# Kernel tuning notes

Measured on AMD Instinct MI355X. Metric: run time of the kernel, lower is better.

Reference implementation:

```python
import jax, jax.numpy as jnp
import numpy as np

N_EMBD = 2048
N_HEAD = 16
HEAD_DIM = N_EMBD // N_HEAD
MAX_SEQ = 2048
ROPE_BASE = 10000.0


def _build_rope_cache(seq_len, head_dim, base):
    theta = 1.0 / (base ** (jnp.arange(0, head_dim, 2, dtype=jnp.float32) / head_dim))
    idx_theta = jnp.arange(seq_len, dtype=jnp.float32)[:, None] * theta[None, :]  # [T, hd/2]
    return jnp.cos(idx_theta), jnp.sin(idx_theta)


def _apply_rope(x, cos, sin):
    # x: [B, T, H, hd]; interleaved (even, odd) pairing along last dim
    B, T, H, hd = x.shape
    xf = x.astype(jnp.float32).reshape(B, T, H, hd // 2, 2)
    x0, x1 = xf[..., 0], xf[..., 1]
    c = cos[None, :T, None, :]
    s = sin[None, :T, None, :]
    out = jnp.stack([x0 * c - x1 * s, x1 * c + x0 * s], axis=-1)
    return out.reshape(B, T, H, hd).astype(x.dtype)


def setup_inputs() -> dict:
    key = jax.random.key(0)
    k1, k2, k3 = jax.random.split(key, 3)
    x = jax.random.normal(k1, (2, 2048, N_EMBD), dtype=jnp.float32)
    # torch Linear(D, 3D, bias=False): y = x @ W.T ; store as [D, 3D] for x @ W
    scale = 1.0 / np.sqrt(N_EMBD)
    w_attn = jax.random.normal(k2, (N_EMBD, 3 * N_EMBD), dtype=jnp.float32) * scale
    w_proj = jax.random.normal(k3, (N_EMBD, N_EMBD), dtype=jnp.float32) * scale
    return {"x": x, "w_attn": w_attn, "w_proj": w_proj}


def reference(x, w_attn, w_proj):
    B, T, D = x.shape
    cos, sin = _build_rope_cache(MAX_SEQ, HEAD_DIM, ROPE_BASE)
    qkv = x @ w_attn                                   # [B, T, 3D]
    q, k, v = jnp.split(qkv, 3, axis=-1)
    q = q.reshape(B, T, N_HEAD, HEAD_DIM)
    k = k.reshape(B, T, N_HEAD, HEAD_DIM)
    v = v.reshape(B, T, N_HEAD, HEAD_DIM)
    q = _apply_rope(q, cos, sin)
    k = _apply_rope(k, cos, sin)
    # non-causal SDPA (original calls F.sdpa without is_causal)
    scale = 1.0 / jnp.sqrt(jnp.asarray(HEAD_DIM, dtype=q.dtype))
    scores = jnp.einsum("bqhd,bkhd->bhqk", q, k) * scale
    attn = jax.nn.softmax(scores, axis=-1)
    y = jnp.einsum("bhqk,bkhd->bqhd", attn, v).reshape(B, T, D)
    return y @ w_proj
```

## Files before the change

kernel.cpp:

```cpp
#include <hip/hip_runtime.h>
#include <cstdint>
#include <cstddef>

typedef __attribute__((ext_vector_type(8))) short bf16x8;
typedef __attribute__((ext_vector_type(8))) unsigned short us8;
typedef __attribute__((ext_vector_type(4))) float f32x4;

#define TSEQ 2048

__device__ __forceinline__ unsigned short f2bf(float f) {
  union { float f; uint32_t u; } v; v.f = f;
  uint32_t u = v.u;
  uint32_t r = (u + 0x7FFFu + ((u >> 16) & 1u)) >> 16;
  return (unsigned short)r;
}
__device__ __forceinline__ unsigned short f2bf_trunc(float f) {
  union { float f; uint32_t u; } v; v.f = f;
  return (unsigned short)(v.u >> 16);
}
__device__ __forceinline__ float bf2f(unsigned short h) {
  union { uint32_t u; float f; } v; v.u = ((uint32_t)h) << 16;
  return v.f;
}

__device__ __forceinline__ void async16(const void* g, void* l) {
  __builtin_amdgcn_global_load_lds(
      (const __attribute__((address_space(1))) unsigned int*)g,
      (__attribute__((address_space(3))) unsigned int*)l,
      16, 0, 0);
}

__global__ __launch_bounds__(256) void cvt_x(
    const float* __restrict__ in, unsigned short* __restrict__ out)
{
  const size_t i = ((size_t)blockIdx.x * 256 + threadIdx.x) * 16;
  f32x4 a0 = *(const f32x4*)(in + i);
  f32x4 a1 = *(const f32x4*)(in + i + 4);
  f32x4 a2 = *(const f32x4*)(in + i + 8);
  f32x4 a3 = *(const f32x4*)(in + i + 12);
  us8 lo, hi;
#pragma unroll
  for (int j = 0; j < 4; j++) {
    lo[j] = f2bf(a0[j]); lo[j + 4] = f2bf(a1[j]);
    hi[j] = f2bf(a2[j]); hi[j + 4] = f2bf(a3[j]);
  }
  *(us8*)(out + i) = lo;
  *(us8*)(out + i + 8) = hi;
}

__global__ __launch_bounds__(256) void transpose_w(
    const float* __restrict__ in, unsigned short* __restrict__ out,
    int R, int C)
{
  __shared__ unsigned short tile[32][33];
  const int bx = blockIdx.x * 32;
  const int by = blockIdx.y * 32;
  const int tx = threadIdx.x & 31;
  const int ty = threadIdx.x >> 5;
#pragma unroll
  for (int r = ty; r < 32; r += 8)
    tile[r][tx] = f2bf(in[(size_t)(by + r) * C + bx + tx]);
  __syncthreads();
#pragma unroll
  for (int r = ty; r < 32; r += 8)
    out[(size_t)(bx + r) * R + by + tx] = tile[tx][r];
}

template <int CF32>
__global__ __launch_bounds__(256) void gemm_bt(
    const unsigned short* __restrict__ A,
    const unsigned short* __restrict__ Bt,
    void* __restrict__ Cv,
    int M, int N, int K, int ldc)
{
  __shared__ unsigned short As[2][128 * 32];
  __shared__ unsigned short Bs[2][128 * 32];
  const int tid  = threadIdx.x;
  const int lane = tid & 63;
  const int w    = tid >> 6;
  const int m0   = blockIdx.y * 128;
  const int n0   = blockIdx.x * 128;
  const int wm   = (w & 1) * 64;
  const int wn   = (w >> 1) * 64;

  const int srow = lane >> 2;
  const int scol = (lane & 3) * 8;
  const unsigned short* ga0 = A  + (size_t)(m0 + w * 16 + srow) * K + scol;
  const unsigned short* ga1 = ga0 + (size_t)64 * K;
  const unsigned short* gb0 = Bt + (size_t)(n0 + w * 16 + srow) * K + scol;
  const unsigned short* gb1 = gb0 + (size_t)64 * K;

  f32x4 acc[4][4];
#pragma unroll
  for (int i = 0; i < 4; i++)
#pragma unroll
    for (int j = 0; j < 4; j++) acc[i][j] = (f32x4){0.f, 0.f, 0.f, 0.f};

  const int frow = lane & 15;
  const int fcol = (lane >> 4) * 8;

  for (int kt = 0; kt < K; kt += 64) {
    __syncthreads();
    async16(ga0 + kt,      &As[0][w * 512]);
    async16(ga1 + kt,      &As[0][(4 + w) * 512]);
    async16(ga0 + kt + 32, &As[1][w * 512]);
    async16(ga1 + kt + 32, &As[1][(4 + w) * 512]);
    async16(gb0 + kt,      &Bs[0][w * 512]);
    async16(gb1 + kt,      &Bs[0][(4 + w) * 512]);
    async16(gb0 + kt + 32, &Bs[1][w * 512]);
    async16(gb1 + kt + 32, &Bs[1][(4 + w) * 512]);
    __syncthreads();

#pragma unroll
    for (int h = 0; h < 2; h++) {
      bf16x8 af[4], bfr[4];
#pragma unroll
      for (int i = 0; i < 4; i++)
        af[i] = *(const bf16x8*)&As[h][(wm + i * 16 + frow) * 32 + fcol];
#pragma unroll
      for (int i = 0; i < 4; i++)
        bfr[i] = *(const bf16x8*)&Bs[h][(wn + i * 16 + frow) * 32 + fcol];
#pragma unroll
      for (int mi = 0; mi < 4; mi++)
#pragma unroll
        for (int ni = 0; ni < 4; ni++)
          acc[mi][ni] = __builtin_amdgcn_mfma_f32_16x16x32_bf16(
              af[mi], bfr[ni], acc[mi][ni], 0, 0, 0);
    }
  }

  const int crow0 = m0 + wm + (lane >> 4) * 4;
  const int ccol0 = n0 + wn + (lane & 15);
  if (CF32) {
    float* Cf = (float*)Cv;
#pragma unroll
    for (int mi = 0; mi < 4; mi++)
#pragma unroll
      for (int i = 0; i < 4; i++) {
        const int row = crow0 + mi * 16 + i;
#pragma unroll
        for (int ni = 0; ni < 4; ni++)
          Cf[(size_t)row * ldc + ccol0 + ni * 16] = acc[mi][ni][i];
      }
  } else {
    unsigned short* Cb = (unsigned short*)Cv;
#pragma unroll
    for (int mi = 0; mi < 4; mi++)
#pragma unroll
      for (int i = 0; i < 4; i++) {
        const int row = crow0 + mi * 16 + i;
#pragma unroll
        for (int ni = 0; ni < 4; ni++)
          Cb[(size_t)row * ldc + ccol0 + ni * 16] = f2bf(acc[mi][ni][i]);
      }
  }
}

__global__ __launch_bounds__(256) void rope_qk(unsigned short* __restrict__ qkv)
{
  const int p   = blockIdx.x * 256 + threadIdx.x;
  const int row = p >> 11;
  const int col = (p & 2047) * 2;
  const int t   = row & (TSEQ - 1);
  const int hd  = col & 127;
  const float theta = exp2f((float)hd * -0.1038102531f);
  const float ang   = (float)t * theta;
  float s, c;
  sincosf(ang, &s, &c);
  const float sc = (col < 2048) ? 0.08838834764831845f : 1.0f;
  uint32_t* ptr = (uint32_t*)(qkv + (size_t)row * 6144 + col);
  const uint32_t u = *ptr;
  const float x0 = bf2f((unsigned short)(u & 0xffffu));
  const float x1 = bf2f((unsigned short)(u >> 16));
  const float o0 = (x0 * c - x1 * s) * sc;
  const float o1 = (x1 * c + x0 * s) * sc;
  *ptr = (uint32_t)f2bf(o0) | ((uint32_t)f2bf(o1) << 16);
}

__global__ __launch_bounds__(256) void repack_v(
    const unsigned short* __restrict__ qkv, unsigned short* __restrict__ Vtg)
{
  __shared__ unsigned short tile[32][33];
  const int tt = blockIdx.x * 32;
  const int dd = blockIdx.y * 32;
  const int bh = blockIdx.z;
  const int b  = bh >> 4, h = bh & 15;
  const int tx = threadIdx.x & 31;
  const int ty = threadIdx.x >> 5;
#pragma unroll
  for (int r = ty; r < 32; r += 8)
    tile[r][tx] = qkv[(size_t)(b * TSEQ + tt + r) * 6144 + 4096 + h * 128 + dd + tx];
  __syncthreads();
#pragma unroll
  for (int r = ty; r < 32; r += 8)
    Vtg[(size_t)bh * 262144 + (size_t)(dd + r) * TSEQ + tt + tx] = tile[tx][r];
}

__global__ __launch_bounds__(256) void attn(
    const unsigned short* __restrict__ qkv,
    const unsigned short* __restrict__ Vtg,
    unsigned short* __restrict__ y)
{
  __shared__ unsigned short Ks[64 * 136];
  __shared__ unsigned short Vs[144 * 72];
  __shared__ unsigned short Ps[4][32 * 72];

  const int tid  = threadIdx.x;
  const int lane = tid & 63;
  const int w    = tid >> 6;
  const int q0   = blockIdx.x * 128;
  const int h    = blockIdx.y;
  const int b    = blockIdx.z;
  const int bh   = b * 16 + h;
  const int quad = lane >> 4;
  const int l15  = lane & 15;
  const int kq   = quad * 8;

  for (int idx = tid; idx < 16 * 72; idx += 256)
    Vs[128 * 72 + idx] = (idx < 72) ? (unsigned short)0x3F80 : (unsigned short)0;

  bf16x8 qa[2][4];
#pragma unroll
  for (int mt = 0; mt < 2; mt++) {
    const unsigned short* gQ =
        qkv + (size_t)(b * TSEQ + q0 + w * 32 + mt * 16 + l15) * 6144 + h * 128 + kq;
#pragma unroll
    for (int dc = 0; dc < 4; dc++) qa[mt][dc] = *(const bf16x8*)(gQ + dc * 32);
  }

  f32x4 ot[2][9];
#pragma unroll
  for (int mt = 0; mt < 2; mt++)
#pragma unroll
    for (int nt = 0; nt < 9; nt++) ot[mt][nt] = (f32x4){0.f, 0.f, 0.f, 0.f};

  const int krow = tid >> 2;
  const int kd   = (tid & 3) * 32;
  const unsigned short* gK = qkv + (size_t)(b * TSEQ) * 6144 + 2048 + h * 128 + kd;
  const int vd = tid >> 1;
  const int vc = (tid & 1) * 32;
  const unsigned short* gVt = Vtg + (size_t)bh * 262144 + (size_t)vd * TSEQ + vc;

  us8 kreg[4], vreg[4];
  {
    const unsigned short* pk = gK + (size_t)krow * 6144;
#pragma unroll
    for (int j = 0; j < 4; j++) kreg[j] = *(const us8*)(pk + j * 8);
#pragma unroll
    for (int j = 0; j < 4; j++) vreg[j] = *(const us8*)(gVt + j * 8);
  }

  for (int kb = 0; kb < TSEQ; kb += 64) {
    __syncthreads();
#pragma unroll
    for (int j = 0; j < 4; j++)
      *(us8*)&Ks[krow * 136 + kd + j * 8] = kreg[j];
#pragma unroll
    for (int j = 0; j < 4; j++)
      *(us8*)&Vs[vd * 72 + vc + j * 8] = vreg[j];
    __syncthreads();

    if (kb + 64 < TSEQ) {
      const unsigned short* pk = gK + (size_t)(kb + 64 + krow) * 6144;
#pragma unroll
      for (int j = 0; j < 4; j++) kreg[j] = *(const us8*)(pk + j * 8);
      const unsigned short* pv = gVt + kb + 64;
#pragma unroll
      for (int j = 0; j < 4; j++) vreg[j] = *(const us8*)(pv + j * 8);
    }

    f32x4 s[2][4];
#pragma unroll
    for (int mt = 0; mt < 2; mt++)
#pragma unroll
      for (int ct = 0; ct < 4; ct++) s[mt][ct] = (f32x4){0.f, 0.f, 0.f, 0.f};
    __builtin_amdgcn_s_setprio(1);
#pragma unroll
    for (int dc = 0; dc < 4; dc++) {
#pragma unroll
      for (int ct = 0; ct < 4; ct++) {
        bf16x8 kf = *(const bf16x8*)&Ks[(ct * 16 + l15) * 136 + dc * 32 + kq];
        s[0][ct] = __builtin_amdgcn_mfma_f32_16x16x32_bf16(qa[0][dc], kf, s[0][ct], 0, 0, 0);
        s[1][ct] = __builtin_amdgcn_mfma_f32_16x16x32_bf16(qa[1][dc], kf, s[1][ct], 0, 0, 0);
      }
    }
    __builtin_amdgcn_s_setprio(0);

    unsigned short* pw = &Ps[w][0];
#pragma unroll
    for (int mt = 0; mt < 2; mt++)
#pragma unroll
      for (int ct = 0; ct < 4; ct++)
#pragma unroll
        for (int i = 0; i < 4; i++)
          pw[(mt * 16 + quad * 4 + i) * 72 + ct * 16 + l15] =
              f2bf_trunc(__expf(fminf(s[mt][ct][i], 30.f)));

    __asm__ volatile("s_waitcnt lgkmcnt(0)" ::: "memory");

    __builtin_amdgcn_s_setprio(1);
#pragma unroll
    for (int kc = 0; kc < 2; kc++) {
      bf16x8 pa0 = *(const bf16x8*)&pw[(l15) * 72 + kc * 32 + kq];
      bf16x8 pa1 = *(const bf16x8*)&pw[(16 + l15) * 72 + kc * 32 + kq];
#pragma unroll
      for (int nt = 0; nt < 9; nt++) {
        bf16x8 vb = *(const bf16x8*)&Vs[(nt * 16 + l15) * 72 + kc * 32 + kq];
        ot[0][nt] = __builtin_amdgcn_mfma_f32_16x16x32_bf16(pa0, vb, ot[0][nt], 0, 0, 0);
        ot[1][nt] = __builtin_amdgcn_mfma_f32_16x16x32_bf16(pa1, vb, ot[1][nt], 0, 0, 0);
      }
    }
    __builtin_amdgcn_s_setprio(0);
  }

#pragma unroll
  for (int mt = 0; mt < 2; mt++) {
    unsigned short* gy =
        y + (size_t)(b * TSEQ + q0 + w * 32 + mt * 16 + quad * 4) * 2048 + h * 128 + l15;
#pragma unroll
    for (int i = 0; i < 4; i++) {
      const float inv = 1.0f / __shfl(ot[mt][8][i], lane & 48);
#pragma unroll
      for (int nt = 0; nt < 8; nt++)
        gy[(size_t)i * 2048 + nt * 16] = f2bf(ot[mt][nt][i] * inv);
    }
  }
}

extern "C" void kernel_launch(void* const* d_in, const int* in_sizes, int n_in,
                              void* d_out, int out_size, void* d_ws, size_t ws_size,
                              hipStream_t stream)
{
  const float* x      = (const float*)d_in[0];
  const float* w_attn = (const float*)d_in[1];
  const float* w_proj = (const float*)d_in[2];

  if (ws_size < 67108864u) return;

  char* ws = (char*)d_ws;
  unsigned short* qkv = (unsigned short*)(ws);
  unsigned short* xb  = (unsigned short*)(ws + 50331648);
  unsigned short* y   = xb;
  unsigned short* wT2 = (unsigned short*)(ws);
  unsigned short* wTa = (unsigned short*)d_out;
  unsigned short* Vtg = (unsigned short*)d_out;

  transpose_w<<<dim3(192, 64), 256, 0, stream>>>(w_attn, wTa, 2048, 6144);
  cvt_x<<<dim3(2048), 256, 0, stream>>>(x, xb);
  gemm_bt<0><<<dim3(48, 32), 256, 0, stream>>>(xb, wTa, (void*)qkv, 4096, 6144, 2048, 6144);
  rope_qk<<<dim3(32768), 256, 0, stream>>>(qkv);
  repack_v<<<dim3(64, 4, 32), 256, 0, stream>>>(qkv, Vtg);
  attn<<<dim3(16, 16, 2), 256, 0, stream>>>(qkv, Vtg, y);
  transpose_w<<<dim3(64, 64), 256, 0, stream>>>(w_proj, wT2, 2048, 2048);
  gemm_bt<1><<<dim3(16, 32), 256, 0, stream>>>(y, wT2, d_out, 4096, 2048, 2048, 2048);
}
```

Before: 428.0 us.

## Fuse RoPE into QKV GEMM epilogue and compute softmax row sums directly

Removes the standalone rope_qk pass by applying rotary embedding and the q scale in the QKV GEMM epilogue. A precomputed cos/sin table is used, and lane pairs exchange values via shuffle. In attention, the extra ones-column MFMA tile used to get the softmax denominator is dropped. Row sums are instead accumulated from the bf16 probabilities with cross-lane reductions, saving a ninth of the PV MFMAs and some LDS. This adds a small table kernel and shuffle/ALU work in the epilogue and the attention loop.

After: 453.9 us. +6.1%, slower.

```diff
diff --git a/kernel.cpp b/kernel.cpp
--- a/kernel.cpp
+++ b/kernel.cpp
@@ -28,6 +28,16 @@
       (const __attribute__((address_space(1))) unsigned int*)g,
       (__attribute__((address_space(3))) unsigned int*)l,
       16, 0, 0);
+}
+
+__global__ __launch_bounds__(256) void rope_table(float2* __restrict__ tbl)
+{
+  const int idx = blockIdx.x * 256 + threadIdx.x;
+  const int t = idx >> 6;
+  const int j = idx & 63;
+  float sn, cs;
+  sincosf((float)t * exp2f((float)j * -0.2076205059273837f), &sn, &cs);
+  tbl[idx] = make_float2(cs, sn);
 }
 
 __global__ __launch_bounds__(256) void cvt_x(
@@ -66,12 +76,13 @@
     out[(size_t)(bx + r) * R + by + tx] = tile[tx][r];
 }
 
-template <int CF32>
+template <int MODE>
 __global__ __launch_bounds__(256) void gemm_bt(
     const unsigned short* __restrict__ A,
     const unsigned short* __restrict__ Bt,
     void* __restrict__ Cv,
-    int M, int N, int K, int ldc)
+    int M, int N, int K, int ldc,
+    const float2* __restrict__ tbl)
 {
   __shared__ unsigned short As[2][128 * 32];
   __shared__ unsigned short Bs[2][128 * 32];
@@ -131,7 +142,7 @@
 
   const int crow0 = m0 + wm + (lane >> 4) * 4;
   const int ccol0 = n0 + wn + (lane & 15);
-  if (CF32) {
+  if (MODE == 1) {
     float* Cf = (float*)Cv;
 #pragma unroll
     for (int mi = 0; mi < 4; mi++)
@@ -144,37 +155,35 @@
       }
   } else {
     unsigned short* Cb = (unsigned short*)Cv;
+    const bool doRope = (n0 < 4096);
+    const float sc = (n0 < 2048) ? 0.08838834764831845f : 1.0f;
+    const int odd = lane & 1;
 #pragma unroll
     for (int mi = 0; mi < 4; mi++)
 #pragma unroll
       for (int i = 0; i < 4; i++) {
         const int row = crow0 + mi * 16 + i;
-#pragma unroll
-        for (int ni = 0; ni < 4; ni++)
-          Cb[(size_t)row * ldc + ccol0 + ni * 16] = f2bf(acc[mi][ni][i]);
-      }
-  }
-}
-
-__global__ __launch_bounds__(256) void rope_qk(unsigned short* __restrict__ qkv)
-{
-  const int p   = blockIdx.x * 256 + threadIdx.x;
-  const int row = p >> 11;
-  const int col = (p & 2047) * 2;
-  const int t   = row & (TSEQ - 1);
-  const int hd  = col & 127;
-  const float theta = exp2f((float)hd * -0.1038102531f);
-  const float ang   = (float)t * theta;
-  float s, c;
-  sincosf(ang, &s, &c);
-  const float sc = (col < 2048) ? 0.08838834764831845f : 1.0f;
-  uint32_t* ptr = (uint32_t*)(qkv + (size_t)row * 6144 + col);
-  const uint32_t u = *ptr;
-  const float x0 = bf2f((unsigned short)(u & 0xffffu));
-  const float x1 = bf2f((unsigned short)(u >> 16));
-  const float o0 = (x0 * c - x1 * s) * sc;
-  const float o1 = (x1 * c + x0 * s) * sc;
-  *ptr = (uint32_t)f2bf(o0) | ((uint32_t)f2bf(o1) << 16);
+        if (doRope) {
+          const size_t tof = (size_t)(row & (TSEQ - 1)) * 64;
+          float2 cs[4];
+#pragma unroll
+          for (int ni = 0; ni < 4; ni++)
+            cs[ni] = tbl[tof + (((ccol0 + ni * 16) & 126) >> 1)];
+#pragma unroll
+          for (int ni = 0; ni < 4; ni++) {
+            const float v = acc[mi][ni][i];
+            const float p = __shfl_xor(v, 1);
+            const float o = (odd ? (v * cs[ni].x + p * cs[ni].y)
+                                 : (v * cs[ni].x - p * cs[ni].y)) * sc;
+            Cb[(size_t)row * ldc + ccol0 + ni * 16] = f2bf(o);
+          }
+        } else {
+#pragma unroll
+          for (int ni = 0; ni < 4; ni++)
+            Cb[(size_t)row * ldc + ccol0 + ni * 16] = f2bf(acc[mi][ni][i]);
+        }
+      }
+  }
 }
 
 __global__ __launch_bounds__(256) void repack_v(
@@ -202,7 +211,7 @@
     unsigned short* __restrict__ y)
 {
   __shared__ unsigned short Ks[64 * 136];
-  __shared__ unsigned short Vs[144 * 72];
+  __shared__ unsigned short Vs[128 * 72];
   __shared__ unsigned short Ps[4][32 * 72];
 
   const int tid  = threadIdx.x;
@@ -216,9 +225,6 @@
   const int l15  = lane & 15;
   const int kq   = quad * 8;
 
-  for (int idx = tid; idx < 16 * 72; idx += 256)
-    Vs[128 * 72 + idx] = (idx < 72) ? (unsigned short)0x3F80 : (unsigned short)0;
-
   bf16x8 qa[2][4];
 #pragma unroll
   for (int mt = 0; mt < 2; mt++) {
@@ -228,11 +234,16 @@
     for (int dc = 0; dc < 4; dc++) qa[mt][dc] = *(const bf16x8*)(gQ + dc * 32);
   }
 
-  f32x4 ot[2][9];
+  f32x4 ot[2][8];
 #pragma unroll
   for (int mt = 0; mt < 2; mt++)
 #pragma unroll
-    for (int nt = 0; nt < 9; nt++) ot[mt][nt] = (f32x4){0.f, 0.f, 0.f, 0.f};
+    for (int nt = 0; nt < 8; nt++) ot[mt][nt] = (f32x4){0.f, 0.f, 0.f, 0.f};
+  float rs[2][4];
+#pragma unroll
+  for (int mt = 0; mt < 2; mt++)
+#pragma unroll
+    for (int i = 0; i < 4; i++) rs[mt][i] = 0.f;
 
   const int krow = tid >> 2;
   const int kd   = (tid & 3) * 32;
@@ -287,14 +298,32 @@
     __builtin_amdgcn_s_setprio(0);
 
     unsigned short* pw = &Ps[w][0];
+    float t8[2][4];
 #pragma unroll
     for (int mt = 0; mt < 2; mt++)
 #pragma unroll
+      for (int i = 0; i < 4; i++) t8[mt][i] = 0.f;
+#pragma unroll
+    for (int mt = 0; mt < 2; mt++)
+#pragma unroll
       for (int ct = 0; ct < 4; ct++)
 #pragma unroll
-        for (int i = 0; i < 4; i++)
-          pw[(mt * 16 + quad * 4 + i) * 72 + ct * 16 + l15] =
-              f2bf_trunc(__expf(fminf(s[mt][ct][i], 30.f)));
+        for (int i = 0; i < 4; i++) {
+          const unsigned short us = f2bf_trunc(__expf(fminf(s[mt][ct][i], 30.f)));
+          pw[(mt * 16 + quad * 4 + i) * 72 + ct * 16 + l15] = us;
+          t8[mt][i] += bf2f(us);
+        }
+#pragma unroll
+    for (int mt = 0; mt < 2; mt++)
+#pragma unroll
+      for (int i = 0; i < 4; i++) {
+        float v = t8[mt][i];
+        v += __shfl_xor(v, 1);
+        v += __shfl_xor(v, 2);
+        v += __shfl_xor(v, 4);
+        v += __shfl_xor(v, 8);
+        rs[mt][i] += v;
+      }
 
     __asm__ volatile("s_waitcnt lgkmcnt(0)" ::: "memory");
 
@@ -304,7 +333,7 @@
       bf16x8 pa0 = *(const bf16x8*)&pw[(l15) * 72 + kc * 32 + kq];
       bf16x8 pa1 = *(const bf16x8*)&pw[(16 + l15) * 72 + kc * 32 + kq];
 #pragma unroll
-      for (int nt = 0; nt < 9; nt++) {
+      for (int nt = 0; nt < 8; nt++) {
         bf16x8 vb = *(const bf16x8*)&Vs[(nt * 16 + l15) * 72 + kc * 32 + kq];
         ot[0][nt] = __builtin_amdgcn_mfma_f32_16x16x32_bf16(pa0, vb, ot[0][nt], 0, 0, 0);
         ot[1][nt] = __builtin_amdgcn_mfma_f32_16x16x32_bf16(pa1, vb, ot[1][nt], 0, 0, 0);
@@ -319,7 +348,7 @@
         y + (size_t)(b * TSEQ + q0 + w * 32 + mt * 16 + quad * 4) * 2048 + h * 128 + l15;
 #pragma unroll
     for (int i = 0; i < 4; i++) {
-      const float inv = 1.0f / __shfl(ot[mt][8][i], lane & 48);
+      const float inv = 1.0f / rs[mt][i];
 #pragma unroll
       for (int nt = 0; nt < 8; nt++)
         gy[(size_t)i * 2048 + nt * 16] = f2bf(ot[mt][nt][i] * inv);
@@ -343,14 +372,15 @@
   unsigned short* y   = xb;
   unsigned short* wT2 = (unsigned short*)(ws);
   unsigned short* wTa = (unsigned short*)d_out;
+  float2* tbl = (float2*)((char*)d_out + 25165824);
   unsigned short* Vtg = (unsigned short*)d_out;
 
   transpose_w<<<dim3(192, 64), 256, 0, stream>>>(w_attn, wTa, 2048, 6144);
+  rope_table<<<dim3(512), 256, 0, stream>>>(tbl);
   cvt_x<<<dim3(2048), 256, 0, stream>>>(x, xb);
-  gemm_bt<0><<<dim3(48, 32), 256, 0, stream>>>(xb, wTa, (void*)qkv, 4096, 6144, 2048, 6144);
-  rope_qk<<<dim3(32768), 256, 0, stream>>>(qkv);
+  gemm_bt<2><<<dim3(48, 32), 256, 0, stream>>>(xb, wTa, (void*)qkv, 4096, 6144, 2048, 6144, tbl);
   repack_v<<<dim3(64, 4, 32), 256, 0, stream>>>(qkv, Vtg);
   attn<<<dim3(16, 16, 2), 256, 0, stream>>>(qkv, Vtg, y);
   transpose_w<<<dim3(64, 64), 256, 0, stream>>>(w_proj, wT2, 2048, 2048);
-  gemm_bt<1><<<dim3(16, 32), 256, 0, stream>>>(y, wT2, d_out, 4096, 2048, 2048, 2048);
-}
+  gemm_bt<1><<<dim3(16, 32), 256, 0, stream>>>(y, wT2, d_out, 4096, 2048, 2048, 2048, nullptr);
+}
```
